# Performance work log

Hardware: AMD Instinct MI355X
Metric: run time of the kernel (lower is better)

The kernel has to match this reference:

```python
import jax, jax.numpy as jnp
import numpy as np

# ---- static config (mirrors YOLOLayer init kwargs) ----
ANCHORS_ALL = jnp.array([[10.,13.],[16.,30.],[33.,23.],[30.,61.],[62.,45.],
                         [59.,119.],[116.,90.],[156.,198.],[373.,326.]], jnp.float32)
MASK = jnp.array([0, 1, 2], jnp.int32)
ANCHORS_PX = ANCHORS_ALL[:3]          # this scale's anchors, pixels
NUM_CLASSES = 1                       # forced by p_boxes.view(..., 6) in _first_loss
IMG_W = IMG_H = 608.0
B, A, GH, GW = 32, 3, 76, 76          # stride-8 head of a 608x608 YOLOv3
T = 48                                # number of ground-truth boxes
IGNORE_THRES = 0.5                    # ignore_thres_first_loss


def _bce(p, t):
    # torch BCELoss clamps log terms at -100
    return -(t * jnp.clip(jnp.log(p), -100.0) + (1.0 - t) * jnp.clip(jnp.log(1.0 - p), -100.0))


def _xywh2xyxy(b):
    xy, wh = b[..., :2], b[..., 2:4]
    return jnp.concatenate([xy - wh / 2, xy + wh / 2], -1)


def setup_inputs() -> dict:
    key = jax.random.key(0)
    k1, k2, k3 = jax.random.split(key, 3)
    x = jax.random.normal(k1, (B, A * (5 + NUM_CLASSES), GH, GW), jnp.float32) * 0.5
    # targets: [image_idx, cx, cy, w, h, cls], normalized coords; ids sorted, first = 0
    img_ids = jnp.sort(jnp.arange(T) % B).astype(jnp.float32)
    xy = jax.random.uniform(k2, (T, 2), minval=0.05, maxval=0.95)
    wh = jax.random.uniform(k3, (T, 2), minval=0.02, maxval=0.30)
    cls = jnp.zeros((T, 1), jnp.float32)
    target = jnp.concatenate([img_ids[:, None], xy, wh, cls], axis=1)
    return {"x": x, "target": target}


def _forward(x, target):
    stride_w, stride_h = IMG_W / GW, IMG_H / GH
    scale_anchors = ANCHORS_PX / jnp.array([stride_w, stride_h], jnp.float32)  # grid units

    pred = x.reshape(B, A, 5 + NUM_CLASSES, GH, GW).transpose(0, 1, 3, 4, 2)   # [B,A,H,W,5+C]
    cx = jax.nn.sigmoid(pred[..., 0]); cy = jax.nn.sigmoid(pred[..., 1])
    pw = pred[..., 2]; ph = pred[..., 3]
    pconf = jax.nn.sigmoid(pred[..., 4]); pcls = jax.nn.sigmoid(pred[..., 5:])

    # ---- __detect: decode boxes to pixel coords ----
    bx = cx + jnp.arange(GW, dtype=jnp.float32)[None, None, None, :]
    by = cy + jnp.arange(GH, dtype=jnp.float32)[None, None, :, None]
    bw = jnp.exp(pw) * scale_anchors[:, 0][None, :, None, None]
    bh = jnp.exp(ph) * scale_anchors[:, 1][None, :, None, None]
    boxes_px = jnp.stack([bx * stride_w, by * stride_h, bw * stride_w, bh * stride_h], -1).reshape(B, -1, 4)
    output = jnp.concatenate([boxes_px, pconf.reshape(B, -1, 1), pcls.reshape(B, -1, NUM_CLASSES)], -1)

    # ---- _first_loss: ignore mask from IoU(decoded preds, GT) in normalized coords ----
    timg = (target[:, 0] - target[0, 0]).astype(jnp.int32)                 # [T]
    tb = target[:, 1:5]                                                    # normalized xywh
    pbn = jnp.stack([bx / GW, by / GH, bw / GW, bh / GH], -1).reshape(B, -1, 4)  # [B,M,4]
    tc = _xywh2xyxy(tb)[:, None, None, :]                                  # [T,1,1,4]
    pc = _xywh2xyxy(pbn)[None]                                             # [1,B,M,4]
    iw = jnp.clip(jnp.minimum(tc[..., 2], pc[..., 2]) - jnp.maximum(tc[..., 0], pc[..., 0]), 0.0)
    ih = jnp.clip(jnp.minimum(tc[..., 3], pc[..., 3]) - jnp.maximum(tc[..., 1], pc[..., 1]), 0.0)
    inter = iw * ih
    ta = (tb[:, 2] * tb[:, 3])[:, None, None]
    pa = (pbn[..., 2] * pbn[..., 3])[None]
    iou = inter / (ta + pa - inter + 1e-16)                                # [T,B,M]
    match = timg[:, None] == jnp.arange(B)[None, :]                        # [T,B] GT-to-image
    best = jnp.max(jnp.where(match[:, :, None], iou, -1.0), 0)             # [B,M]
    ignore_mask = (best <= IGNORE_THRES).astype(jnp.float32).reshape(B, A, GH, GW)

    # ---- __build_target ----
    gxy = tb[:, :2] * jnp.array([GW, GH], jnp.float32)
    gwh = tb[:, 2:4] * jnp.array([GW, GH], jnp.float32)
    gwh_n = tb[:, 2:4]
    label = target[:, 5].astype(jnp.int32)
    an = ANCHORS_ALL / jnp.array([IMG_W, IMG_H], jnp.float32)              # [9,2] normalized
    w_inter = jnp.minimum(an[:, 0:1], gwh_n[None, :, 0]) * jnp.minimum(an[:, 1:2], gwh_n[None, :, 1])
    w_union = (an[:, 0] * an[:, 1] + 1e-16)[:, None] + (gwh_n[:, 0] * gwh_n[:, 1])[None, :] - w_inter
    anc_iou = w_inter / w_union                                            # [9,T]
    best_idx = jnp.argmax(anc_iou, 0)                                      # [T]
    gi = gxy[:, 0].astype(jnp.int32); gj = gxy[:, 1].astype(jnp.int32)
    in_mask = jnp.any(best_idx[:, None] == MASK[None, :], 1)
    valid = in_mask & (gi < GW) & (gj < GH) & (gi >= 0) & (gj >= 0)
    bi = best_idx - MASK[0]
    sc = 2.0 - gwh_n[:, 0] * gwh_n[:, 1]
    img_s = jnp.where(valid, timg, B)          # invalid rows -> OOB batch idx, dropped by scatter
    idx = (img_s, bi, gj, gi)

    z = jnp.zeros((B, A, GH, GW), jnp.float32)
    obj = z.at[idx].set(1.0, mode='drop')
    noobj = jnp.ones((B, A, GH, GW), jnp.float32).at[idx].set(0.0, mode='drop')
    tx = z.at[idx].set(gxy[:, 0] - jnp.floor(gxy[:, 0]), mode='drop')
    ty = z.at[idx].set(gxy[:, 1] - jnp.floor(gxy[:, 1]), mode='drop')
    tw = z.at[idx].set(jnp.log(gwh[:, 0] * stride_w / ANCHORS_PX[bi, 0] + 1e-16), mode='drop')
    th = z.at[idx].set(jnp.log(gwh[:, 1] * stride_h / ANCHORS_PX[bi, 1] + 1e-16), mode='drop')
    tconf = obj
    tcls = jnp.zeros((B, A, GH, GW, NUM_CLASSES), jnp.float32).at[img_s, bi, gj, gi, label].set(1.0, mode='drop')
    scale = jnp.ones((B, A, GH, GW), jnp.float32).at[idx].set(sc, mode='drop')

    # ignore_mask[obj==1] = 1 ; noobj_mask[ignore_mask==0] = 0
    ignore = jnp.where(obj > 0, 1.0, ignore_mask)
    noobj = jnp.where(ignore == 0, 0.0, noobj)

    s2 = scale * scale
    loss_x = jnp.sum(obj * (cx - tx) ** 2 * s2)
    loss_y = jnp.sum(obj * (cy - ty) ** 2 * s2)
    loss_w = jnp.sum(obj * (pw - tw) ** 2 * s2)
    loss_h = jnp.sum(obj * (ph - th) ** 2 * s2)
    loss_conf_obj = jnp.sum(obj * _bce(pconf, tconf))
    loss_conf_noobj = jnp.sum(noobj * _bce(pconf, tconf))
    loss_cls = jnp.sum(obj[..., None] * _bce(pcls, tcls))
    loss_conf = loss_conf_obj + loss_conf_noobj
    total = loss_x + loss_y + loss_w + loss_h + loss_conf + loss_cls
    r = lambda v: jnp.reshape(v, (1,))
    return (output, r(total), r(loss_x + loss_y), r(loss_w + loss_h), r(loss_conf), r(loss_cls))


def reference(x, target):
    return _forward(x, target)
```

## Files before the change

kernel.cpp:

```cpp
#include <hip/hip_runtime.h>

#define NB 32
#define NA 3
#define NGH 76
#define NGW 76
#define NT 48
#define PLANE (NGH * NGW)
#define NCELL (NB * NA * PLANE)
#define NOUT  (NCELL * 6)
#define CPT 4
#define BLK 128
#define NTHREAD (NCELL / CPT)
#define NBLK2 (NTHREAD / BLK)

static_assert(NTHREAD % BLK == 0, "grid must divide evenly");
static_assert(PLANE % CPT == 0, "4 consecutive cells stay in one plane row-chunk");


__launch_bounds__(BLK)
__global__ void yolo_main(const float* __restrict__ x,
                          const float* __restrict__ tgt,
                          float* __restrict__ out,
                          float4* __restrict__ partials) {
    __shared__ float st[NT * 16];
    __shared__ unsigned long long sball[NB];
    __shared__ int soff[NB + 1];
    __shared__ int sord[NT];

    const int tx  = threadIdx.x;
    const int tid = blockIdx.x * BLK + tx;
    const int g   = tid * CPT;

    const int gw0 = g % NGW;
    const int gh  = (g / NGW) % NGH;
    const int a   = (g / PLANE) % NA;
    const int b   = g / (NA * PLANE);

    const float* xp = x + (size_t)(b * (NA * 6) + a * 6) * PLANE + (g % PLANE);
    const float4 v0 = *(const float4*)(xp);
    const float4 v1 = *(const float4*)(xp + PLANE);
    const float4 v2 = *(const float4*)(xp + 2 * PLANE);
    const float4 v3 = *(const float4*)(xp + 3 * PLANE);
    const float4 v4 = *(const float4*)(xp + 4 * PLANE);
    const float4 v5 = *(const float4*)(xp + 5 * PLANE);

    if (tx < 64) {
        const int t = tx;
        const bool isT = (t < NT);
        int timg = 999;
        if (isT) {
            const float t00 = tgt[0];
            const float* tr = tgt + t * 6;
            timg = (int)(tr[0] - t00);
            const float bxn = tr[1], byn = tr[2], bwn = tr[3], bhn = tr[4];

            const float gx = bxn * (float)NGW;
            const float gy = byn * (float)NGH;
            const int gi = (int)gx;
            const int gj = (int)gy;
            const float tarea = bwn * bhn;

            const float aw_px[9] = {10.f,16.f,33.f,30.f,62.f,59.f,116.f,156.f,373.f};
            const float ah_px[9] = {13.f,30.f,23.f,61.f,45.f,119.f,90.f,198.f,326.f};
            int bidx = 0; float biou = -1e30f;
            #pragma unroll
            for (int k = 0; k < 9; ++k) {
                const float aw = aw_px[k] / 608.0f;
                const float ah = ah_px[k] / 608.0f;
                const float wi = fminf(aw, bwn) * fminf(ah, bhn);
                const float un = ((aw * ah + 1e-16f) + tarea) - wi;
                const float iou = wi / un;
                if (iou > biou) { biou = iou; bidx = k; }
            }
            const bool inm = (bidx >= 0) && (bidx <= 2);
            const bool valid = inm && (gi < NGW) && (gj < NGH) && (gi >= 0) && (gj >= 0);
            const int bic = bidx < 0 ? 0 : (bidx > 2 ? 2 : bidx);
            const float apw = (bic == 0) ? 10.f : ((bic == 1) ? 16.f : 33.f);
            const float aph = (bic == 0) ? 13.f : ((bic == 1) ? 30.f : 23.f);

            float* s = st + t * 16;
            s[0]  = (float)timg;
            s[1]  = valid ? 1.0f : 0.0f;
            s[2]  = (float)bidx;
            s[3]  = (float)gj;
            s[4]  = (float)gi;
            s[5]  = gx - floorf(gx);
            s[6]  = gy - floorf(gy);
            s[7]  = __logf(((bwn * (float)NGW) * 8.0f) / apw + 1e-16f);
            s[8]  = __logf(((bhn * (float)NGH) * 8.0f) / aph + 1e-16f);
            s[9]  = 2.0f - bwn * bhn;
            s[10] = bxn - bwn * 0.5f;
            s[11] = byn - bhn * 0.5f;
            s[12] = bxn + bwn * 0.5f;
            s[13] = byn + bhn * 0.5f;
            s[14] = tarea;
            s[15] = 0.0f;
        }

        int cnt = 0;
        for (int bb = 0; bb < NB; ++bb) {
            const unsigned long long m = __ballot(timg == bb);
            if (t == 0) sball[bb] = m;
            if (t == bb) cnt = (int)__popcll(m);
        }
        int inc = cnt;
        #pragma unroll
        for (int d = 1; d < 32; d <<= 1) {
            const int v = __shfl_up(inc, d);
            if (t >= d) inc += v;
        }
        if (t < NB) soff[t] = inc - cnt;
        if (t == NB - 1) soff[NB] = inc;
        if (isT) {
            const unsigned long long m = sball[timg];
            const int rank = (int)__popcll(m & ((1ULL << t) - 1ULL));
            sord[soff[timg] + rank] = t;
        }
    }

    const float p0[CPT] = {v0.x, v0.y, v0.z, v0.w};
    const float p1[CPT] = {v1.x, v1.y, v1.z, v1.w};
    const float p2[CPT] = {v2.x, v2.y, v2.z, v2.w};
    const float p3[CPT] = {v3.x, v3.y, v3.z, v3.w};
    const float p4[CPT] = {v4.x, v4.y, v4.z, v4.w};
    const float p5[CPT] = {v5.x, v5.y, v5.z, v5.w};

    const float sa_w = (a == 0) ? 1.25f  : ((a == 1) ? 2.0f  : 4.125f);
    const float sa_h = (a == 0) ? 1.625f : ((a == 1) ? 3.75f : 2.875f);

    float cxv[CPT], cyv[CPT], pcf[CPT], pcl[CPT];
    float px1[CPT], py1[CPT], px2[CPT], py2[CPT], par[CPT];
    float o24[CPT * 6];

    #pragma unroll
    for (int c = 0; c < CPT; ++c) {
        const float cx    = 1.0f / (1.0f + __expf(-p0[c]));
        const float cy    = 1.0f / (1.0f + __expf(-p1[c]));
        const float pconf = 1.0f / (1.0f + __expf(-p4[c]));
        const float pcls  = 1.0f / (1.0f + __expf(-p5[c]));
        const float bx = cx + (float)(gw0 + c);
        const float by = cy + (float)gh;
        const float bw = __expf(p2[c]) * sa_w;
        const float bh = __expf(p3[c]) * sa_h;

        o24[c * 6 + 0] = bx * 8.0f;
        o24[c * 6 + 1] = by * 8.0f;
        o24[c * 6 + 2] = bw * 8.0f;
        o24[c * 6 + 3] = bh * 8.0f;
        o24[c * 6 + 4] = pconf;
        o24[c * 6 + 5] = pcls;

        const float pxc = bx * (1.0f / NGW), pyc = by * (1.0f / NGH);
        const float pwn = bw * (1.0f / NGW), phn = bh * (1.0f / NGH);
        cxv[c] = cx; cyv[c] = cy; pcf[c] = pconf; pcl[c] = pcls;
        px1[c] = pxc - pwn * 0.5f; py1[c] = pyc - phn * 0.5f;
        px2[c] = pxc + pwn * 0.5f; py2[c] = pyc + phn * 0.5f;
        par[c] = pwn * phn;
    }

    {
        float4* ob = (float4*)(out + (size_t)g * 6);
        #pragma unroll
        for (int k = 0; k < 6; ++k)
            ob[k] = make_float4(o24[4 * k], o24[4 * k + 1], o24[4 * k + 2], o24[4 * k + 3]);
    }

    __syncthreads();

    float best[CPT] = {-1.f, -1.f, -1.f, -1.f};
    int   so[CPT]   = {-1, -1, -1, -1};
    {
        const int j1 = soff[b + 1];
        for (int j = soff[b]; j < j1; ++j) {
            const int t = sord[j];
            const float* s = st + t * 16;
            const float s1 = s[1], s2f = s[2], s3f = s[3], s4f = s[4];
            const float x1 = s[10], y1 = s[11], x2 = s[12], y2 = s[13], ta = s[14];
            const bool vmatch = (s1 != 0.0f) && ((int)s2f == a) && ((int)s3f == gh);
            #pragma unroll
            for (int c = 0; c < CPT; ++c) {
                const float iw = fmaxf(fminf(x2, px2[c]) - fmaxf(x1, px1[c]), 0.0f);
                const float ih = fmaxf(fminf(y2, py2[c]) - fmaxf(y1, py1[c]), 0.0f);
                const float inter = iw * ih;
                const float iou = inter / (((ta + par[c]) - inter) + 1e-16f);
                if (iou > best[c]) best[c] = iou;
                if (vmatch && ((int)s4f == gw0 + c)) so[c] = t;
            }
        }
    }

    float lxy = 0.f, lwh = 0.f, lconf = 0.f, lcls = 0.f;
    #pragma unroll
    for (int c = 0; c < CPT; ++c) {
        if (so[c] >= 0) {
            const float* s = st + so[c] * 16;
            const float sc = s[9], s2 = sc * sc;
            const float dx = cxv[c] - s[5], dy = cyv[c] - s[6];
            const float dw = p2[c] - s[7], dh = p3[c] - s[8];
            lxy   += (dx * dx + dy * dy) * s2;
            lwh   += (dw * dw + dh * dh) * s2;
            lconf += -fmaxf(__logf(pcf[c]), -100.0f);
            lcls  += -fmaxf(__logf(pcl[c]), -100.0f);
        } else if (best[c] <= 0.5f) {
            lconf += -fmaxf(__logf(1.0f - pcf[c]), -100.0f);
        }
    }

    #pragma unroll
    for (int off = 32; off > 0; off >>= 1) {
        lxy   += __shfl_down(lxy, off);
        lwh   += __shfl_down(lwh, off);
        lconf += __shfl_down(lconf, off);
        lcls  += __shfl_down(lcls, off);
    }
    __shared__ float red[2][4];
    const int lane = tx & 63, wv = tx >> 6;
    if (lane == 0) { red[wv][0] = lxy; red[wv][1] = lwh; red[wv][2] = lconf; red[wv][3] = lcls; }
    __syncthreads();
    if (tx == 0) {
        partials[blockIdx.x] = make_float4(red[0][0] + red[1][0], red[0][1] + red[1][1],
                                           red[0][2] + red[1][2], red[0][3] + red[1][3]);
    }
}

__launch_bounds__(256)
__global__ void yolo_final(const float4* __restrict__ partials,
                           float* __restrict__ lossbuf) {
    float a0 = 0.f, a1 = 0.f, a2 = 0.f, a3 = 0.f;
    for (int i = threadIdx.x; i < NBLK2; i += 256) {
        const float4 p = partials[i];
        a0 += p.x; a1 += p.y; a2 += p.z; a3 += p.w;
    }
    #pragma unroll
    for (int off = 32; off > 0; off >>= 1) {
        a0 += __shfl_down(a0, off);
        a1 += __shfl_down(a1, off);
        a2 += __shfl_down(a2, off);
        a3 += __shfl_down(a3, off);
    }
    __shared__ float red[4][4];
    const int lane = threadIdx.x & 63, wv = threadIdx.x >> 6;
    if (lane == 0) { red[wv][0] = a0; red[wv][1] = a1; red[wv][2] = a2; red[wv][3] = a3; }
    __syncthreads();
    if (threadIdx.x == 0) {
        float s0 = 0.f, s1 = 0.f, s2 = 0.f, s3 = 0.f;
        #pragma unroll
        for (int w = 0; w < 4; ++w) { s0 += red[w][0]; s1 += red[w][1]; s2 += red[w][2]; s3 += red[w][3]; }
        lossbuf[1] = s0;
        lossbuf[2] = s1;
        lossbuf[3] = s2;
        lossbuf[4] = s3;
        lossbuf[0] = ((s0 + s1) + s2) + s3;
    }
}

extern "C" void kernel_launch(void* const* d_in, const int* in_sizes, int n_in,
                              void* d_out, int out_size, void* d_ws, size_t ws_size,
                              hipStream_t stream) {
    const float* x   = (const float*)d_in[0];
    const float* tgt = (const float*)d_in[1];
    float* out      = (float*)d_out;
    float4* partial = (float4*)d_ws;

    hipLaunchKernelGGL(yolo_main,  dim3(NBLK2), dim3(BLK), 0, stream, x, tgt, out, partial);
    hipLaunchKernelGGL(yolo_final, dim3(1),     dim3(256), 0, stream, partial, out + NOUT);
    (void)in_sizes; (void)n_in; (void)out_size; (void)ws_size;
}
```

Before: 17.21 us.

## Fuse final loss reduction into main kernel via per-block completion flags

Removes the separate single-block reduction kernel. Each block now writes its partial sums plus a magic-value flag, and block 0 spins on all flags before reducing the partials and writing the loss scalars. This saves a kernel launch and the dependency gap between the two kernels. The block size also goes from 128 to 192, and the output stores become nontemporal vector stores. The flags are never cleared, so on repeated calls block 0 may read stale partials from a previous call, and the spin relies on block 0 not starving the other blocks.

```diff
diff --git a/kernel.cpp b/kernel.cpp
--- a/kernel.cpp
+++ b/kernel.cpp
@@ -9,26 +9,33 @@
 #define NCELL (NB * NA * PLANE)
 #define NOUT  (NCELL * 6)
 #define CPT 4
-#define BLK 128
+#define BLK 192
 #define NTHREAD (NCELL / CPT)
-#define NBLK2 (NTHREAD / BLK)
+#define NBLKS (NTHREAD / BLK)
+#define MAGIC 0x59A10C47u
 
 static_assert(NTHREAD % BLK == 0, "grid must divide evenly");
 static_assert(PLANE % CPT == 0, "4 consecutive cells stay in one plane row-chunk");
 
+typedef float f4 __attribute__((ext_vector_type(4)));
+
 
 __launch_bounds__(BLK)
-__global__ void yolo_main(const float* __restrict__ x,
-                          const float* __restrict__ tgt,
-                          float* __restrict__ out,
-                          float4* __restrict__ partials) {
+__global__ void yolo_fused(const float* __restrict__ x,
+                           const float* __restrict__ tgt,
+                           float* __restrict__ out,
+                           float* __restrict__ partials,
+                           unsigned int* __restrict__ flags,
+                           float* __restrict__ lossbuf) {
     __shared__ float st[NT * 16];
     __shared__ unsigned long long sball[NB];
     __shared__ int soff[NB + 1];
     __shared__ int sord[NT];
+    __shared__ float red[3][4];
 
     const int tx  = threadIdx.x;
-    const int tid = blockIdx.x * BLK + tx;
+    const int bid = blockIdx.x;
+    const int tid = bid * BLK + tx;
     const int g   = tid * CPT;
 
     const int gw0 = g % NGW;
@@ -37,12 +44,12 @@
     const int b   = g / (NA * PLANE);
 
     const float* xp = x + (size_t)(b * (NA * 6) + a * 6) * PLANE + (g % PLANE);
-    const float4 v0 = *(const float4*)(xp);
-    const float4 v1 = *(const float4*)(xp + PLANE);
-    const float4 v2 = *(const float4*)(xp + 2 * PLANE);
-    const float4 v3 = *(const float4*)(xp + 3 * PLANE);
-    const float4 v4 = *(const float4*)(xp + 4 * PLANE);
-    const float4 v5 = *(const float4*)(xp + 5 * PLANE);
+    const f4 v0 = *(const f4*)(xp);
+    const f4 v1 = *(const f4*)(xp + PLANE);
+    const f4 v2 = *(const f4*)(xp + 2 * PLANE);
+    const f4 v3 = *(const f4*)(xp + 3 * PLANE);
+    const f4 v4 = *(const f4*)(xp + 4 * PLANE);
+    const f4 v5 = *(const f4*)(xp + 5 * PLANE);
 
     if (tx < 64) {
         const int t = tx;
@@ -130,7 +137,8 @@
 
     float cxv[CPT], cyv[CPT], pcf[CPT], pcl[CPT];
     float px1[CPT], py1[CPT], px2[CPT], py2[CPT], par[CPT];
-    float o24[CPT * 6];
+    f4 o0, o1, o2, o3, o4, o5;
+    float* o24[6] = {(float*)&o0, (float*)&o1, (float*)&o2, (float*)&o3, (float*)&o4, (float*)&o5};
 
     #pragma unroll
     for (int c = 0; c < CPT; ++c) {
@@ -143,12 +151,13 @@
         const float bw = __expf(p2[c]) * sa_w;
         const float bh = __expf(p3[c]) * sa_h;
 
-        o24[c * 6 + 0] = bx * 8.0f;
-        o24[c * 6 + 1] = by * 8.0f;
-        o24[c * 6 + 2] = bw * 8.0f;
-        o24[c * 6 + 3] = bh * 8.0f;
-        o24[c * 6 + 4] = pconf;
-        o24[c * 6 + 5] = pcls;
+        const int j0 = c * 6;
+        o24[j0 / 4][j0 % 4]             = bx * 8.0f;
+        o24[(j0 + 1) / 4][(j0 + 1) % 4] = by * 8.0f;
+        o24[(j0 + 2) / 4][(j0 + 2) % 4] = bw * 8.0f;
+        o24[(j0 + 3) / 4][(j0 + 3) % 4] = bh * 8.0f;
+        o24[(j0 + 4) / 4][(j0 + 4) % 4] = pconf;
+        o24[(j0 + 5) / 4][(j0 + 5) % 4] = pcls;
 
         const float pxc = bx * (1.0f / NGW), pyc = by * (1.0f / NGH);
         const float pwn = bw * (1.0f / NGW), phn = bh * (1.0f / NGH);
@@ -159,10 +168,13 @@
     }
 
     {
-        float4* ob = (float4*)(out + (size_t)g * 6);
-        #pragma unroll
-        for (int k = 0; k < 6; ++k)
-            ob[k] = make_float4(o24[4 * k], o24[4 * k + 1], o24[4 * k + 2], o24[4 * k + 3]);
+        f4* ob = (f4*)(out + (size_t)g * 6);
+        __builtin_nontemporal_store(o0, ob + 0);
+        __builtin_nontemporal_store(o1, ob + 1);
+        __builtin_nontemporal_store(o2, ob + 2);
+        __builtin_nontemporal_store(o3, ob + 3);
+        __builtin_nontemporal_store(o4, ob + 4);
+        __builtin_nontemporal_store(o5, ob + 5);
     }
 
     __syncthreads();
@@ -213,44 +225,58 @@
         lconf += __shfl_down(lconf, off);
         lcls  += __shfl_down(lcls, off);
     }
-    __shared__ float red[2][4];
     const int lane = tx & 63, wv = tx >> 6;
     if (lane == 0) { red[wv][0] = lxy; red[wv][1] = lwh; red[wv][2] = lconf; red[wv][3] = lcls; }
     __syncthreads();
     if (tx == 0) {
-        partials[blockIdx.x] = make_float4(red[0][0] + red[1][0], red[0][1] + red[1][1],
-                                           red[0][2] + red[1][2], red[0][3] + red[1][3]);
-    }
-}
-
-__launch_bounds__(256)
-__global__ void yolo_final(const float4* __restrict__ partials,
-                           float* __restrict__ lossbuf) {
-    float a0 = 0.f, a1 = 0.f, a2 = 0.f, a3 = 0.f;
-    for (int i = threadIdx.x; i < NBLK2; i += 256) {
-        const float4 p = partials[i];
-        a0 += p.x; a1 += p.y; a2 += p.z; a3 += p.w;
-    }
-    #pragma unroll
-    for (int off = 32; off > 0; off >>= 1) {
-        a0 += __shfl_down(a0, off);
-        a1 += __shfl_down(a1, off);
-        a2 += __shfl_down(a2, off);
-        a3 += __shfl_down(a3, off);
-    }
-    __shared__ float red[4][4];
-    const int lane = threadIdx.x & 63, wv = threadIdx.x >> 6;
-    if (lane == 0) { red[wv][0] = a0; red[wv][1] = a1; red[wv][2] = a2; red[wv][3] = a3; }
-    __syncthreads();
-    if (threadIdx.x == 0) {
-        float s0 = 0.f, s1 = 0.f, s2 = 0.f, s3 = 0.f;
+        f4 p;
+        p.x = red[0][0] + red[1][0] + red[2][0];
+        p.y = red[0][1] + red[1][1] + red[2][1];
+        p.z = red[0][2] + red[1][2] + red[2][2];
+        p.w = red[0][3] + red[1][3] + red[2][3];
+        *(f4*)(partials + bid * 4) = p;
+        __threadfence();
+        __hip_atomic_store(&flags[bid], MAGIC, __ATOMIC_RELAXED, __HIP_MEMORY_SCOPE_AGENT);
+    }
+
+    if (bid == 0) {
+        for (;;) {
+            int ok = 1;
+            for (int i = tx; i < NBLKS; i += BLK) {
+                if (__hip_atomic_load(&flags[i], __ATOMIC_RELAXED, __HIP_MEMORY_SCOPE_AGENT) != MAGIC) {
+                    ok = 0; break;
+                }
+            }
+            if (__syncthreads_and(ok)) break;
+            __builtin_amdgcn_s_sleep(1);
+        }
+        __threadfence();
+
+        float a0 = 0.f, a1 = 0.f, a2 = 0.f, a3 = 0.f;
+        for (int i = tx; i < NBLKS; i += BLK) {
+            const f4 p = *(const f4*)(partials + i * 4);
+            a0 += p.x; a1 += p.y; a2 += p.z; a3 += p.w;
+        }
         #pragma unroll
-        for (int w = 0; w < 4; ++w) { s0 += red[w][0]; s1 += red[w][1]; s2 += red[w][2]; s3 += red[w][3]; }
-        lossbuf[1] = s0;
-        lossbuf[2] = s1;
-        lossbuf[3] = s2;
-        lossbuf[4] = s3;
-        lossbuf[0] = ((s0 + s1) + s2) + s3;
+        for (int off = 32; off > 0; off >>= 1) {
+            a0 += __shfl_down(a0, off);
+            a1 += __shfl_down(a1, off);
+            a2 += __shfl_down(a2, off);
+            a3 += __shfl_down(a3, off);
+        }
+        if (lane == 0) { red[wv][0] = a0; red[wv][1] = a1; red[wv][2] = a2; red[wv][3] = a3; }
+        __syncthreads();
+        if (tx == 0) {
+            const float s0 = red[0][0] + red[1][0] + red[2][0];
+            const float s1 = red[0][1] + red[1][1] + red[2][1];
+            const float s2 = red[0][2] + red[1][2] + red[2][2];
+            const float s3 = red[0][3] + red[1][3] + red[2][3];
+            lossbuf[1] = s0;
+            lossbuf[2] = s1;
+            lossbuf[3] = s2;
+            lossbuf[4] = s3;
+            lossbuf[0] = ((s0 + s1) + s2) + s3;
+        }
     }
 }
 
@@ -259,10 +285,12 @@
                               hipStream_t stream) {
     const float* x   = (const float*)d_in[0];
     const float* tgt = (const float*)d_in[1];
-    float* out      = (float*)d_out;
-    float4* partial = (float4*)d_ws;
-
-    hipLaunchKernelGGL(yolo_main,  dim3(NBLK2), dim3(BLK), 0, stream, x, tgt, out, partial);
-    hipLaunchKernelGGL(yolo_final, dim3(1),     dim3(256), 0, stream, partial, out + NOUT);
+    float* out          = (float*)d_out;
+    float* lossbuf      = out + NOUT;
+    float* partials     = (float*)d_ws;
+    unsigned int* flags = (unsigned int*)(partials + NBLKS * 4);
+
+    hipLaunchKernelGGL(yolo_fused, dim3(NBLKS), dim3(BLK), 0, stream,
+                       x, tgt, out, partials, flags, lossbuf);
     (void)in_sizes; (void)n_in; (void)out_size; (void)ws_size;
 }
```

After: 53.14 us. 3.09x slower.

## Fuse final loss reduction into main kernel via flag-polling last reducer

Applied to the files above, without the earlier changes.

Drops the separate single-block reduction kernel. Each block now publishes its four partial sums, then sets a per-block flag with a magic value. Block 0 spins on all flags and does the final reduction inside the same launch, which saves one kernel launch and the gap between launches. The flags are never reset between calls, so on later calls block 0 may read stale partials from the previous run. The scheme also relies on every block being co-resident or able to make progress while block 0 spins.

```diff
diff --git a/kernel.cpp b/kernel.cpp
--- a/kernel.cpp
+++ b/kernel.cpp
@@ -11,24 +11,31 @@
 #define CPT 4
 #define BLK 128
 #define NTHREAD (NCELL / CPT)
-#define NBLK2 (NTHREAD / BLK)
+#define NBLKS (NTHREAD / BLK)
+#define MAGIC 0x59A10C47u
 
 static_assert(NTHREAD % BLK == 0, "grid must divide evenly");
 static_assert(PLANE % CPT == 0, "4 consecutive cells stay in one plane row-chunk");
+
+typedef float f4 __attribute__((ext_vector_type(4)));
 
 
 __launch_bounds__(BLK)
 __global__ void yolo_main(const float* __restrict__ x,
                           const float* __restrict__ tgt,
                           float* __restrict__ out,
-                          float4* __restrict__ partials) {
+                          float* __restrict__ partials,
+                          unsigned int* __restrict__ flags,
+                          float* __restrict__ lossbuf) {
     __shared__ float st[NT * 16];
     __shared__ unsigned long long sball[NB];
     __shared__ int soff[NB + 1];
     __shared__ int sord[NT];
+    __shared__ float red[2][4];
 
     const int tx  = threadIdx.x;
-    const int tid = blockIdx.x * BLK + tx;
+    const int bid = blockIdx.x;
+    const int tid = bid * BLK + tx;
     const int g   = tid * CPT;
 
     const int gw0 = g % NGW;
@@ -213,44 +220,57 @@
         lconf += __shfl_down(lconf, off);
         lcls  += __shfl_down(lcls, off);
     }
-    __shared__ float red[2][4];
     const int lane = tx & 63, wv = tx >> 6;
     if (lane == 0) { red[wv][0] = lxy; red[wv][1] = lwh; red[wv][2] = lconf; red[wv][3] = lcls; }
     __syncthreads();
     if (tx == 0) {
-        partials[blockIdx.x] = make_float4(red[0][0] + red[1][0], red[0][1] + red[1][1],
-                                           red[0][2] + red[1][2], red[0][3] + red[1][3]);
-    }
-}
-
-__launch_bounds__(256)
-__global__ void yolo_final(const float4* __restrict__ partials,
-                           float* __restrict__ lossbuf) {
-    float a0 = 0.f, a1 = 0.f, a2 = 0.f, a3 = 0.f;
-    for (int i = threadIdx.x; i < NBLK2; i += 256) {
-        const float4 p = partials[i];
-        a0 += p.x; a1 += p.y; a2 += p.z; a3 += p.w;
-    }
-    #pragma unroll
-    for (int off = 32; off > 0; off >>= 1) {
-        a0 += __shfl_down(a0, off);
-        a1 += __shfl_down(a1, off);
-        a2 += __shfl_down(a2, off);
-        a3 += __shfl_down(a3, off);
-    }
-    __shared__ float red[4][4];
-    const int lane = threadIdx.x & 63, wv = threadIdx.x >> 6;
-    if (lane == 0) { red[wv][0] = a0; red[wv][1] = a1; red[wv][2] = a2; red[wv][3] = a3; }
-    __syncthreads();
-    if (threadIdx.x == 0) {
-        float s0 = 0.f, s1 = 0.f, s2 = 0.f, s3 = 0.f;
+        __hip_atomic_store(&partials[bid * 4 + 0], red[0][0] + red[1][0], __ATOMIC_RELAXED, __HIP_MEMORY_SCOPE_AGENT);
+        __hip_atomic_store(&partials[bid * 4 + 1], red[0][1] + red[1][1], __ATOMIC_RELAXED, __HIP_MEMORY_SCOPE_AGENT);
+        __hip_atomic_store(&partials[bid * 4 + 2], red[0][2] + red[1][2], __ATOMIC_RELAXED, __HIP_MEMORY_SCOPE_AGENT);
+        __hip_atomic_store(&partials[bid * 4 + 3], red[0][3] + red[1][3], __ATOMIC_RELAXED, __HIP_MEMORY_SCOPE_AGENT);
+        asm volatile("s_waitcnt vmcnt(0)" ::: "memory");
+        __hip_atomic_store(&flags[bid], MAGIC, __ATOMIC_RELAXED, __HIP_MEMORY_SCOPE_AGENT);
+    }
+
+    if (bid == 0) {
+        for (;;) {
+            int ok = 1;
+            for (int i = tx; i < NBLKS; i += BLK) {
+                if (__hip_atomic_load(&flags[i], __ATOMIC_RELAXED, __HIP_MEMORY_SCOPE_AGENT) != MAGIC) {
+                    ok = 0; break;
+                }
+            }
+            if (__syncthreads_and(ok)) break;
+            __builtin_amdgcn_s_sleep(8);
+        }
+
+        float a0 = 0.f, a1 = 0.f, a2 = 0.f, a3 = 0.f;
+        for (int i = tx; i < NBLKS; i += BLK) {
+            a0 += __hip_atomic_load(&partials[i * 4 + 0], __ATOMIC_RELAXED, __HIP_MEMORY_SCOPE_AGENT);
+            a1 += __hip_atomic_load(&partials[i * 4 + 1], __ATOMIC_RELAXED, __HIP_MEMORY_SCOPE_AGENT);
+            a2 += __hip_atomic_load(&partials[i * 4 + 2], __ATOMIC_RELAXED, __HIP_MEMORY_SCOPE_AGENT);
+            a3 += __hip_atomic_load(&partials[i * 4 + 3], __ATOMIC_RELAXED, __HIP_MEMORY_SCOPE_AGENT);
+        }
         #pragma unroll
-        for (int w = 0; w < 4; ++w) { s0 += red[w][0]; s1 += red[w][1]; s2 += red[w][2]; s3 += red[w][3]; }
-        lossbuf[1] = s0;
-        lossbuf[2] = s1;
-        lossbuf[3] = s2;
-        lossbuf[4] = s3;
-        lossbuf[0] = ((s0 + s1) + s2) + s3;
+        for (int off = 32; off > 0; off >>= 1) {
+            a0 += __shfl_down(a0, off);
+            a1 += __shfl_down(a1, off);
+            a2 += __shfl_down(a2, off);
+            a3 += __shfl_down(a3, off);
+        }
+        if (lane == 0) { red[wv][0] = a0; red[wv][1] = a1; red[wv][2] = a2; red[wv][3] = a3; }
+        __syncthreads();
+        if (tx == 0) {
+            const float s0 = red[0][0] + red[1][0];
+            const float s1 = red[0][1] + red[1][1];
+            const float s2 = red[0][2] + red[1][2];
+            const float s3 = red[0][3] + red[1][3];
+            lossbuf[1] = s0;
+            lossbuf[2] = s1;
+            lossbuf[3] = s2;
+            lossbuf[4] = s3;
+            lossbuf[0] = ((s0 + s1) + s2) + s3;
+        }
     }
 }
 
@@ -259,10 +279,12 @@
                               hipStream_t stream) {
     const float* x   = (const float*)d_in[0];
     const float* tgt = (const float*)d_in[1];
-    float* out      = (float*)d_out;
-    float4* partial = (float4*)d_ws;
-
-    hipLaunchKernelGGL(yolo_main,  dim3(NBLK2), dim3(BLK), 0, stream, x, tgt, out, partial);
-    hipLaunchKernelGGL(yolo_final, dim3(1),     dim3(256), 0, stream, partial, out + NOUT);
+    float* out          = (float*)d_out;
+    float* lossbuf      = out + NOUT;
+    float* partials     = (float*)d_ws;
+    unsigned int* flags = (unsigned int*)(partials + NBLKS * 4);
+
+    hipLaunchKernelGGL(yolo_main, dim3(NBLKS), dim3(BLK), 0, stream,
+                       x, tgt, out, partials, flags, lossbuf);
     (void)in_sizes; (void)n_in; (void)out_size; (void)ws_size;
 }
```

After: 19.95 us. +15.9%, slower.
